# Optimization experiments

Measured on AMD Instinct MI355X. Metric: run time of the kernel, lower is better.

The kernel has to match this reference:

```python
import jax, jax.numpy as jnp
from jax import lax
import numpy as np

S, N, E = 4, 50000, 800000
D_IN, D_NOISE, D_H, D_OUT = 96, 32, 32, 128
F_CAT = D_IN + D_NOISE + D_H  # 160, matches nn.Linear(input_dim+noise_dim+32, out)


def setup_inputs() -> dict:
    key = jax.random.key(0)
    ks = jax.random.split(key, 8)
    X = jax.random.normal(ks[0], (1, N, D_IN), dtype=jnp.float32)
    h = jax.random.normal(ks[1], (1, N, D_H), dtype=jnp.float32)
    # Bernoulli(0.5) noise, sampled in setup for determinism (original samples in forward)
    epsilon = (jax.random.uniform(ks[2], (S, N, D_NOISE)) < 0.5).astype(jnp.float32)
    W = jax.random.normal(ks[3], (F_CAT, D_OUT), dtype=jnp.float32) * 0.02
    b = jnp.zeros((D_OUT,), dtype=jnp.float32)
    gin_eps = jnp.zeros((), dtype=jnp.float32)  # init_eps=0, learn_eps=True
    src = jax.random.randint(ks[4], (E,), 0, N, dtype=jnp.int32)
    dst = jax.random.randint(ks[5], (E,), 0, N, dtype=jnp.int32)
    return {"X": X, "h": h, "epsilon": epsilon, "W": W, "b": b,
            "gin_eps": gin_eps, "src": src, "dst": dst}


def reference(X, h, epsilon, W, b, gin_eps, src, dst):
    # X: [1,N,D_IN] expanded to sample_size; h: [1,N,32] expanded; epsilon: [S,N,D_NOISE]
    s, n = epsilon.shape[0], X.shape[1]
    Xb = jnp.broadcast_to(X, (s, n, X.shape[2]))
    hb = jnp.broadcast_to(h, (s, n, h.shape[2]))
    x_all = jnp.concatenate([Xb, epsilon, hb], axis=2)  # [S,N,F_CAT]

    def per_sample(carry, x):  # x: [N,F_CAT]
        # GINConv('sum'): (1+eps)*x + sum_{j in N(i)} x_j, then Linear, then activation
        agg = (1.0 + gin_eps) * x + jax.ops.segment_sum(x[src], dst, num_segments=n)
        y = jax.nn.relu(agg @ W + b)           # [N,D_OUT]
        return carry, jnp.mean(y, axis=0)      # per-layer mean over nodes -> [D_OUT]

    _, means = lax.scan(per_sample, None, x_all)  # [S,D_OUT]
    # outputTensor[i] = tempdim12 broadcasts the [D_OUT] vector over the node axis
    out = jnp.broadcast_to(means[:, None, :], (s, n, W.shape[1]))
    return jax.nn.relu(out), epsilon
```

## Files before the change

### kernel.cpp

```cpp
#include <hip/hip_runtime.h>

#define N_NODES  50000
#define N_EDGES  800000
#define D_OUTF   128
#define F_PACK   256
#define NTILES   3125
#define GEMM_BLOCKS 512
#define NB1      196
#define PBX 12500
#define PBB 25000
#define PBZ 196
#define PB_TOT (PBX + PBB + PBZ)

typedef __attribute__((ext_vector_type(8))) short bf16x8;
typedef __attribute__((ext_vector_type(4))) float f32x4;

__device__ __forceinline__ unsigned short f2bf(float x) {
  unsigned int u = __float_as_uint(x);
  u += 0x7FFFu + ((u >> 16) & 1u);
  return (unsigned short)(u >> 16);
}
__device__ __forceinline__ float bflo(unsigned int u) { return __uint_as_float(u << 16); }
__device__ __forceinline__ float bfhi(unsigned int u) { return __uint_as_float(u & 0xFFFF0000u); }
__device__ __forceinline__ unsigned int pack2(float a, float b) {
  return (unsigned int)f2bf(a) | ((unsigned int)f2bf(b) << 16);
}
__device__ __forceinline__ unsigned int spreadLo(unsigned int rep) {
  return (((rep & 0x08040201u) + 0x7F7F7F7Fu) >> 7) & 0x01010101u;
}
__device__ __forceinline__ unsigned int spreadHi(unsigned int rep) {
  return (((rep & 0x80402010u) + 0x7F7F7F7Fu) >> 7) & 0x01010101u;
}

__global__ void k_pack(const float* __restrict__ X, const float* __restrict__ h,
                       const float* __restrict__ eps,
                       unsigned int* __restrict__ featXH,
                       unsigned int* __restrict__ epsb, int* __restrict__ cnt) {
  int blk = blockIdx.x, tid = threadIdx.x;
  if (blk < PBX) {
    int t = blk * 256 + tid;
    int node = t >> 6, f = (t & 63) << 1;
    float a, c;
    if (f < 96) { a = X[node * 96 + f];      c = X[node * 96 + f + 1]; }
    else        { a = h[node * 32 + f - 96]; c = h[node * 32 + f - 95]; }
    featXH[t] = pack2(a, c);
  } else if (blk < PBX + PBB) {
    long g = (long)(blk - PBX) * 256 + tid;
    float v = eps[g];
    unsigned long long m = __ballot(v > 0.5f);
    int lane = tid & 63;
    if ((lane & 31) == 0) {
      long idx = g >> 5;
      int s = (int)(idx / N_NODES);
      int node = (int)(idx - (long)s * N_NODES);
      epsb[node * 4 + s] = (unsigned int)(m >> ((lane >> 5) * 32));
    }
  } else {
    int i = (blk - PBX - PBB) * 256 + tid;
    if (i < N_NODES) cnt[i] = 0;
  }
}

__global__ void k_hist(const int* __restrict__ dst, int* __restrict__ cnt) {
  int i = blockIdx.x * blockDim.x + threadIdx.x;
  if (i < N_EDGES) atomicAdd(&cnt[dst[i]], 1);
}

__global__ void k_scan1(const int* __restrict__ cnt, int* __restrict__ excl,
                        int* __restrict__ bsum) {
  __shared__ int wpart[4];
  int tid = threadIdx.x, lane = tid & 63, wid = tid >> 6;
  int i = blockIdx.x * 256 + tid;
  int v = (i < N_NODES) ? cnt[i] : 0;
  int x = v;
#pragma unroll
  for (int d = 1; d < 64; d <<= 1) {
    int t = __shfl_up(x, d, 64);
    if (lane >= d) x += t;
  }
  if (lane == 63) wpart[wid] = x;
  __syncthreads();
  if (tid == 0) {
    int s = 0;
#pragma unroll
    for (int w = 0; w < 4; ++w) { int t = wpart[w]; wpart[w] = s; s += t; }
    bsum[blockIdx.x] = s;
  }
  __syncthreads();
  if (i < N_NODES) excl[i] = wpart[wid] + x - v;
}

__global__ void k_scan2(const int* __restrict__ bsum, int* __restrict__ boff) {
  __shared__ int sd[256];
  int tid = threadIdx.x;
  int v = (tid < NB1) ? bsum[tid] : 0;
  sd[tid] = v;
  __syncthreads();
  for (int d = 1; d < 256; d <<= 1) {
    int t = (tid >= d) ? sd[tid - d] : 0;
    __syncthreads();
    sd[tid] += t;
    __syncthreads();
  }
  if (tid < NB1) boff[tid] = sd[tid] - v;
}

__global__ void k_scan3(int* __restrict__ off, const int* __restrict__ boff,
                        int* __restrict__ cursor) {
  int i = blockIdx.x * 256 + threadIdx.x;
  if (i < N_NODES) {
    int o = off[i] + boff[blockIdx.x];
    off[i] = o;
    cursor[i] = o;
  }
  if (i == 0) off[N_NODES] = N_EDGES;
}

__global__ void k_scatter(const int* __restrict__ src, const int* __restrict__ dst,
                          int* __restrict__ cursor, int* __restrict__ csr) {
  int i = blockIdx.x * blockDim.x + threadIdx.x;
  if (i < N_EDGES) {
    int pos = atomicAdd(&cursor[dst[i]], 1);
    csr[pos] = src[i];
  }
}

__global__ __launch_bounds__(256) void k_agg16(
    const uint4* __restrict__ feat4, const unsigned int* __restrict__ epsw,
    const float* __restrict__ geps_p, const int* __restrict__ off,
    const int* __restrict__ csr, uint4* __restrict__ agg4) {
  int gt = blockIdx.x * blockDim.x + threadIdx.x;
  int n  = gt >> 4;
  int li = gt & 15;
  if (n >= N_NODES) return;
  float ge = 1.0f + geps_p[0];
  int wsel = li >> 2, bsh = (li & 3) * 8;

  uint4 sf = feat4[n * 16 + li];
  float af0 = ge * bflo(sf.x), af1 = ge * bfhi(sf.x);
  float af2 = ge * bflo(sf.y), af3 = ge * bfhi(sf.y);
  float af4 = ge * bflo(sf.z), af5 = ge * bfhi(sf.z);
  float af6 = ge * bflo(sf.w), af7 = ge * bfhi(sf.w);
  unsigned int Bself = (epsw[n * 4 + wsel] >> bsh) & 0xFFu;
  unsigned int accLo = 0, accHi = 0;

  int e = off[n], e1 = off[n + 1];
  for (; e + 1 < e1; e += 2) {
    int s0 = csr[e], s1 = csr[e + 1];
    uint4 f0 = feat4[s0 * 16 + li];
    uint4 f1 = feat4[s1 * 16 + li];
    unsigned int w0 = epsw[s0 * 4 + wsel];
    unsigned int w1 = epsw[s1 * 4 + wsel];
    af0 += bflo(f0.x) + bflo(f1.x);  af1 += bfhi(f0.x) + bfhi(f1.x);
    af2 += bflo(f0.y) + bflo(f1.y);  af3 += bfhi(f0.y) + bfhi(f1.y);
    af4 += bflo(f0.z) + bflo(f1.z);  af5 += bfhi(f0.z) + bfhi(f1.z);
    af6 += bflo(f0.w) + bflo(f1.w);  af7 += bfhi(f0.w) + bfhi(f1.w);
    unsigned int B0 = (w0 >> bsh) & 0xFFu;
    unsigned int B1 = (w1 >> bsh) & 0xFFu;
    unsigned int r0 = B0 | (B0 << 8);  r0 |= r0 << 16;
    unsigned int r1 = B1 | (B1 << 8);  r1 |= r1 << 16;
    accLo += spreadLo(r0) + spreadLo(r1);
    accHi += spreadHi(r0) + spreadHi(r1);
  }
  if (e < e1) {
    int s0 = csr[e];
    uint4 f0 = feat4[s0 * 16 + li];
    unsigned int w0 = epsw[s0 * 4 + wsel];
    af0 += bflo(f0.x); af1 += bfhi(f0.x);
    af2 += bflo(f0.y); af3 += bfhi(f0.y);
    af4 += bflo(f0.z); af5 += bfhi(f0.z);
    af6 += bflo(f0.w); af7 += bfhi(f0.w);
    unsigned int B0 = (w0 >> bsh) & 0xFFu;
    unsigned int r0 = B0 | (B0 << 8);  r0 |= r0 << 16;
    accLo += spreadLo(r0);
    accHi += spreadHi(r0);
  }

  float ev0 = ge * (float)(Bself & 1u)        + (float)(accLo & 0xFFu);
  float ev1 = ge * (float)((Bself >> 1) & 1u) + (float)((accLo >> 8) & 0xFFu);
  float ev2 = ge * (float)((Bself >> 2) & 1u) + (float)((accLo >> 16) & 0xFFu);
  float ev3 = ge * (float)((Bself >> 3) & 1u) + (float)((accLo >> 24) & 0xFFu);
  float ev4 = ge * (float)((Bself >> 4) & 1u) + (float)(accHi & 0xFFu);
  float ev5 = ge * (float)((Bself >> 5) & 1u) + (float)((accHi >> 8) & 0xFFu);
  float ev6 = ge * (float)((Bself >> 6) & 1u) + (float)((accHi >> 16) & 0xFFu);
  float ev7 = ge * (float)((Bself >> 7) & 1u) + (float)((accHi >> 24) & 0xFFu);

  uint4 oXh, oEp;
  oXh.x = pack2(af0, af1); oXh.y = pack2(af2, af3);
  oXh.z = pack2(af4, af5); oXh.w = pack2(af6, af7);
  oEp.x = pack2(ev0, ev1); oEp.y = pack2(ev2, ev3);
  oEp.z = pack2(ev4, ev5); oEp.w = pack2(ev6, ev7);
  agg4[n * 32 + li]      = oXh;
  agg4[n * 32 + 16 + li] = oEp;
}

__global__ __launch_bounds__(256) void k_gemm(const unsigned short* __restrict__ agg,
    const float* __restrict__ W, const float* __restrict__ b,
    float* __restrict__ partials) {
  int tid = threadIdx.x;
  int lane = tid & 63;
  int w = tid >> 6;
  int col = lane & 15;
  int quad = lane >> 4;

  bf16x8 Bsh[2][4];
  bf16x8 Bep[2];
  float bias[2];
#pragma unroll
  for (int i = 0; i < 2; ++i) {
    int obase = (2 * w + i) * 16;
    bias[i] = b[obase + col];
#pragma unroll
    for (int kb = 0; kb < 4; ++kb) {
      bf16x8 f;
#pragma unroll
      for (int j = 0; j < 8; ++j) {
        int k = kb * 32 + quad * 8 + j;
        int wr = (k < 96) ? k : k + 32;
        f[j] = (short)f2bf(W[wr * D_OUTF + obase + col]);
      }
      Bsh[i][kb] = f;
    }
    bf16x8 g;
#pragma unroll
    for (int j = 0; j < 8; ++j)
      g[j] = (short)f2bf(W[(96 + quad * 8 + j) * D_OUTF + obase + col]);
    Bep[i] = g;
  }

  f32x4 psum[4][2];
#pragma unroll
  for (int s = 0; s < 4; ++s)
#pragma unroll
    for (int i = 0; i < 2; ++i) psum[s][i] = (f32x4){0.f, 0.f, 0.f, 0.f};

  for (int t = blockIdx.x; t < NTILES; t += gridDim.x) {
    const unsigned short* arow = agg + (long)(t * 16 + col) * F_PACK;
    bf16x8 Ash[4];
#pragma unroll
    for (int kb = 0; kb < 4; ++kb)
      Ash[kb] = *(const bf16x8*)(arow + kb * 32 + quad * 8);
    f32x4 csh[2];
    csh[0] = (f32x4){0.f, 0.f, 0.f, 0.f};
    csh[1] = (f32x4){0.f, 0.f, 0.f, 0.f};
#pragma unroll
    for (int kb = 0; kb < 4; ++kb) {
      csh[0] = __builtin_amdgcn_mfma_f32_16x16x32_bf16(Ash[kb], Bsh[0][kb], csh[0], 0, 0, 0);
      csh[1] = __builtin_amdgcn_mfma_f32_16x16x32_bf16(Ash[kb], Bsh[1][kb], csh[1], 0, 0, 0);
    }
#pragma unroll
    for (int s = 0; s < 4; ++s) {
      bf16x8 Aep = *(const bf16x8*)(arow + 128 + s * 32 + quad * 8);
#pragma unroll
      for (int i = 0; i < 2; ++i) {
        f32x4 c = __builtin_amdgcn_mfma_f32_16x16x32_bf16(Aep, Bep[i], csh[i], 0, 0, 0);
#pragma unroll
        for (int r = 0; r < 4; ++r)
          psum[s][i][r] += fmaxf(c[r] + bias[i], 0.f);
      }
    }
  }

#pragma unroll
  for (int s = 0; s < 4; ++s)
#pragma unroll
    for (int i = 0; i < 2; ++i) {
      float v = psum[s][i][0] + psum[s][i][1] + psum[s][i][2] + psum[s][i][3];
      v += __shfl_xor(v, 16, 64);
      v += __shfl_xor(v, 32, 64);
      if (quad == 0)
        partials[blockIdx.x * 512 + s * 128 + (2 * w + i) * 16 + col] = v;
    }
}

__global__ void k_reduce(const float* __restrict__ partials, float* __restrict__ means) {
  int idx = blockIdx.x * 64 + threadIdx.x;
  float t = 0.f;
  for (int blk = 0; blk < GEMM_BLOCKS; ++blk) t += partials[blk * 512 + idx];
  means[idx] = fmaxf(t * (1.0f / (float)N_NODES), 0.f);
}

#define OUT0_F4 6400000L
#define EPS_F4  1600000L
__global__ void k_out(const float* __restrict__ means, const float* __restrict__ eps,
                      float* __restrict__ out) {
  long i = (long)blockIdx.x * blockDim.x + threadIdx.x;
  if (i < OUT0_F4) {
    int o4 = (int)(i & 31);
    long sn = i >> 5;
    int s = (int)(sn / N_NODES);
    ((float4*)out)[i] = ((const float4*)means)[s * 32 + o4];
  } else if (i < OUT0_F4 + EPS_F4) {
    long j = i - OUT0_F4;
    ((float4*)out)[OUT0_F4 + j] = ((const float4*)eps)[j];
  }
}

extern "C" void kernel_launch(void* const* d_in, const int* in_sizes, int n_in,
                              void* d_out, int out_size, void* d_ws, size_t ws_size,
                              hipStream_t stream) {
  const float* X    = (const float*)d_in[0];
  const float* h    = (const float*)d_in[1];
  const float* eps  = (const float*)d_in[2];
  const float* W    = (const float*)d_in[3];
  const float* b    = (const float*)d_in[4];
  const float* geps = (const float*)d_in[5];
  const int*   src  = (const int*)d_in[6];
  const int*   dst  = (const int*)d_in[7];
  float* out = (float*)d_out;

  char* w = (char*)d_ws;
  unsigned int*  featXH = (unsigned int*)w;  w += (size_t)N_NODES * 64 * 4;
  unsigned int*  epsb   = (unsigned int*)w;  w += (size_t)N_NODES * 4 * 4;
  unsigned int*  agg_u  = (unsigned int*)w;  w += (size_t)N_NODES * 128 * 4;
  int*   off      = (int*)w;   w += (size_t)(N_NODES + 16) * 4;
  int*   cnt      = (int*)w;   w += (size_t)N_NODES * 4;
  int*   cursor   = (int*)w;   w += (size_t)N_NODES * 4;
  int*   csr      = (int*)w;   w += (size_t)N_EDGES * 4;
  int*   bsum     = (int*)w;   w += 256 * 4;
  int*   boff     = (int*)w;   w += 256 * 4;
  float* partials = (float*)w; w += (size_t)GEMM_BLOCKS * 512 * 4;
  float* means    = (float*)w; w += 512 * 4;

  int eb = (N_EDGES + 255) / 256;
  k_pack<<<PB_TOT, 256, 0, stream>>>(X, h, eps, featXH, epsb, cnt);
  k_hist<<<eb, 256, 0, stream>>>(dst, cnt);
  k_scan1<<<NB1, 256, 0, stream>>>(cnt, off, bsum);
  k_scan2<<<1, 256, 0, stream>>>(bsum, boff);
  k_scan3<<<NB1, 256, 0, stream>>>(off, boff, cursor);
  k_scatter<<<eb, 256, 0, stream>>>(src, dst, cursor, csr);

  k_agg16<<<NTILES, 256, 0, stream>>>((const uint4*)featXH, epsb,
                                      geps, off, csr, (uint4*)agg_u);

  k_gemm<<<GEMM_BLOCKS, 256, 0, stream>>>((const unsigned short*)agg_u, W, b, partials);
  k_reduce<<<8, 64, 0, stream>>>(partials, means);

  long total_f4 = OUT0_F4 + EPS_F4;
  k_out<<<(int)((total_f4 + 255) / 256), 256, 0, stream>>>(means, eps, out);
}
```

Before: 355.1 us.

## Fuse aggregation and MFMA GEMM via LDS, prepack W fragments, parallelize reduce

The GIN aggregation kernel now keeps each 16-node tile of aggregated bf16 features in shared memory and runs the MFMA linear+ReLU+sum directly, so the 25 MB aggregated-feature buffer is no longer written to and re-read from global memory. W is converted to bf16 MFMA fragment layout once in the prep kernel, and every block loads its fragments with vector loads. The reduce step now sums 3125 transposed per-block partials using one wavefront per output with shuffles. The cost is a per-block W fragment reload and a larger partials buffer.

After: 356.2 us. About the same (+0.3%).

```diff
diff --git a/kernel.cpp b/kernel.cpp
--- a/kernel.cpp
+++ b/kernel.cpp
@@ -2,15 +2,14 @@
 
 #define N_NODES  50000
 #define N_EDGES  800000
-#define D_OUTF   128
-#define F_PACK   256
 #define NTILES   3125
-#define GEMM_BLOCKS 512
+#define PT_STRIDE 3200
 #define NB1      196
 #define PBX 12500
 #define PBB 25000
+#define PBW 40
 #define PBZ 196
-#define PB_TOT (PBX + PBB + PBZ)
+#define PB_TOT (PBX + PBB + PBW + PBZ)
 
 typedef __attribute__((ext_vector_type(8))) short bf16x8;
 typedef __attribute__((ext_vector_type(4))) float f32x4;
@@ -32,10 +31,10 @@
   return (((rep & 0x80402010u) + 0x7F7F7F7Fu) >> 7) & 0x01010101u;
 }
 
-__global__ void k_pack(const float* __restrict__ X, const float* __restrict__ h,
-                       const float* __restrict__ eps,
-                       unsigned int* __restrict__ featXH,
-                       unsigned int* __restrict__ epsb, int* __restrict__ cnt) {
+__global__ void k_prep(const float* __restrict__ X, const float* __restrict__ h,
+                       const float* __restrict__ eps, const float* __restrict__ W,
+                       unsigned int* __restrict__ featXH, unsigned int* __restrict__ epsb,
+                       unsigned int* __restrict__ Wfrag, int* __restrict__ cnt) {
   int blk = blockIdx.x, tid = threadIdx.x;
   if (blk < PBX) {
     int t = blk * 256 + tid;
@@ -55,8 +54,25 @@
       int node = (int)(idx - (long)s * N_NODES);
       epsb[node * 4 + s] = (unsigned int)(m >> ((lane >> 5) * 32));
     }
+  } else if (blk < PBX + PBB + PBW) {
+    int u = (blk - PBX - PBB) * 256 + tid;
+    if (u < 10240) {
+      int flat = u * 2;
+      int qj = flat & 31;
+      int c  = (flat >> 5) & 127;
+      int kb = flat >> 12;
+      int q = qj >> 3, j = qj & 7;
+      int wr0;
+      if (kb < 4) {
+        int k = kb * 32 + q * 8 + j;
+        wr0 = (k < 96) ? k : k + 32;
+      } else {
+        wr0 = 96 + q * 8 + j;
+      }
+      Wfrag[u] = pack2(W[wr0 * 128 + c], W[(wr0 + 1) * 128 + c]);
+    }
   } else {
-    int i = (blk - PBX - PBB) * 256 + tid;
+    int i = (blk - PBX - PBB - PBW) * 256 + tid;
     if (i < N_NODES) cnt[i] = 0;
   }
 }
@@ -125,14 +141,18 @@
   }
 }
 
-__global__ __launch_bounds__(256) void k_agg16(
+__global__ __launch_bounds__(256) void k_fused(
     const uint4* __restrict__ feat4, const unsigned int* __restrict__ epsw,
+    const unsigned short* __restrict__ Wf, const float* __restrict__ b,
     const float* __restrict__ geps_p, const int* __restrict__ off,
-    const int* __restrict__ csr, uint4* __restrict__ agg4) {
-  int gt = blockIdx.x * blockDim.x + threadIdx.x;
-  int n  = gt >> 4;
-  int li = gt & 15;
-  if (n >= N_NODES) return;
+    const int* __restrict__ csr, float* __restrict__ partialsT) {
+  __shared__ __align__(16) unsigned short lds[16 * 264];
+  int tid = threadIdx.x;
+  int lane = tid & 63;
+  int w = tid >> 6;
+  int li = tid & 15;
+  int r = tid >> 4;
+  int n = blockIdx.x * 16 + r;
   float ge = 1.0f + geps_p[0];
   int wsel = li >> 2, bsh = (li & 3) * 8;
 
@@ -190,94 +210,59 @@
   oXh.z = pack2(af4, af5); oXh.w = pack2(af6, af7);
   oEp.x = pack2(ev0, ev1); oEp.y = pack2(ev2, ev3);
   oEp.z = pack2(ev4, ev5); oEp.w = pack2(ev6, ev7);
-  agg4[n * 32 + li]      = oXh;
-  agg4[n * 32 + 16 + li] = oEp;
-}
-
-__global__ __launch_bounds__(256) void k_gemm(const unsigned short* __restrict__ agg,
-    const float* __restrict__ W, const float* __restrict__ b,
-    float* __restrict__ partials) {
-  int tid = threadIdx.x;
-  int lane = tid & 63;
-  int w = tid >> 6;
-  int col = lane & 15;
-  int quad = lane >> 4;
-
-  bf16x8 Bsh[2][4];
-  bf16x8 Bep[2];
+  unsigned short* rp = lds + r * 264;
+  *(uint4*)(rp + li * 8) = oXh;
+  *(uint4*)(rp + 128 + li * 8) = oEp;
+  __syncthreads();
+
+  int col = li, quad = lane >> 4;
+  bf16x8 Bsh[2][4], Bep[2];
   float bias[2];
 #pragma unroll
   for (int i = 0; i < 2; ++i) {
-    int obase = (2 * w + i) * 16;
-    bias[i] = b[obase + col];
-#pragma unroll
-    for (int kb = 0; kb < 4; ++kb) {
-      bf16x8 f;
-#pragma unroll
-      for (int j = 0; j < 8; ++j) {
-        int k = kb * 32 + quad * 8 + j;
-        int wr = (k < 96) ? k : k + 32;
-        f[j] = (short)f2bf(W[wr * D_OUTF + obase + col]);
-      }
-      Bsh[i][kb] = f;
-    }
-    bf16x8 g;
-#pragma unroll
-    for (int j = 0; j < 8; ++j)
-      g[j] = (short)f2bf(W[(96 + quad * 8 + j) * D_OUTF + obase + col]);
-    Bep[i] = g;
-  }
-
-  f32x4 psum[4][2];
-#pragma unroll
-  for (int s = 0; s < 4; ++s)
-#pragma unroll
-    for (int i = 0; i < 2; ++i) psum[s][i] = (f32x4){0.f, 0.f, 0.f, 0.f};
-
-  for (int t = blockIdx.x; t < NTILES; t += gridDim.x) {
-    const unsigned short* arow = agg + (long)(t * 16 + col) * F_PACK;
-    bf16x8 Ash[4];
+    int c = (2 * w + i) * 16 + col;
+    bias[i] = b[c];
 #pragma unroll
     for (int kb = 0; kb < 4; ++kb)
-      Ash[kb] = *(const bf16x8*)(arow + kb * 32 + quad * 8);
-    f32x4 csh[2];
-    csh[0] = (f32x4){0.f, 0.f, 0.f, 0.f};
-    csh[1] = (f32x4){0.f, 0.f, 0.f, 0.f};
-#pragma unroll
-    for (int kb = 0; kb < 4; ++kb) {
-      csh[0] = __builtin_amdgcn_mfma_f32_16x16x32_bf16(Ash[kb], Bsh[0][kb], csh[0], 0, 0, 0);
-      csh[1] = __builtin_amdgcn_mfma_f32_16x16x32_bf16(Ash[kb], Bsh[1][kb], csh[1], 0, 0, 0);
-    }
-#pragma unroll
-    for (int s = 0; s < 4; ++s) {
-      bf16x8 Aep = *(const bf16x8*)(arow + 128 + s * 32 + quad * 8);
-#pragma unroll
-      for (int i = 0; i < 2; ++i) {
-        f32x4 c = __builtin_amdgcn_mfma_f32_16x16x32_bf16(Aep, Bep[i], csh[i], 0, 0, 0);
-#pragma unroll
-        for (int r = 0; r < 4; ++r)
-          psum[s][i][r] += fmaxf(c[r] + bias[i], 0.f);
-      }
-    }
-  }
-
-#pragma unroll
-  for (int s = 0; s < 4; ++s)
+      Bsh[i][kb] = *(const bf16x8*)(Wf + (kb * 128 + c) * 32 + quad * 8);
+    Bep[i] = *(const bf16x8*)(Wf + (4 * 128 + c) * 32 + quad * 8);
+  }
+
+  const unsigned short* ap = lds + col * 264;
+  f32x4 csh[2];
+  csh[0] = (f32x4){0.f, 0.f, 0.f, 0.f};
+  csh[1] = (f32x4){0.f, 0.f, 0.f, 0.f};
+#pragma unroll
+  for (int kb = 0; kb < 4; ++kb) {
+    bf16x8 Ash = *(const bf16x8*)(ap + kb * 32 + quad * 8);
+    csh[0] = __builtin_amdgcn_mfma_f32_16x16x32_bf16(Ash, Bsh[0][kb], csh[0], 0, 0, 0);
+    csh[1] = __builtin_amdgcn_mfma_f32_16x16x32_bf16(Ash, Bsh[1][kb], csh[1], 0, 0, 0);
+  }
+#pragma unroll
+  for (int s = 0; s < 4; ++s) {
+    bf16x8 Aep = *(const bf16x8*)(ap + 128 + s * 32 + quad * 8);
 #pragma unroll
     for (int i = 0; i < 2; ++i) {
-      float v = psum[s][i][0] + psum[s][i][1] + psum[s][i][2] + psum[s][i][3];
+      f32x4 c = __builtin_amdgcn_mfma_f32_16x16x32_bf16(Aep, Bep[i], csh[i], 0, 0, 0);
+      float v = fmaxf(c[0] + bias[i], 0.f) + fmaxf(c[1] + bias[i], 0.f)
+              + fmaxf(c[2] + bias[i], 0.f) + fmaxf(c[3] + bias[i], 0.f);
       v += __shfl_xor(v, 16, 64);
       v += __shfl_xor(v, 32, 64);
       if (quad == 0)
-        partials[blockIdx.x * 512 + s * 128 + (2 * w + i) * 16 + col] = v;
+        partialsT[(long)(s * 128 + (2 * w + i) * 16 + col) * PT_STRIDE + blockIdx.x] = v;
     }
-}
-
-__global__ void k_reduce(const float* __restrict__ partials, float* __restrict__ means) {
-  int idx = blockIdx.x * 64 + threadIdx.x;
+  }
+}
+
+__global__ void k_reduce(const float* __restrict__ partialsT, float* __restrict__ means) {
+  int wid = (blockIdx.x * 256 + threadIdx.x) >> 6;
+  int lane = threadIdx.x & 63;
+  const float* row = partialsT + (long)wid * PT_STRIDE;
   float t = 0.f;
-  for (int blk = 0; blk < GEMM_BLOCKS; ++blk) t += partials[blk * 512 + idx];
-  means[idx] = fmaxf(t * (1.0f / (float)N_NODES), 0.f);
+  for (int i = lane; i < NTILES; i += 64) t += row[i];
+#pragma unroll
+  for (int d = 1; d < 64; d <<= 1) t += __shfl_xor(t, d, 64);
+  if (lane == 0) means[wid] = fmaxf(t * (1.0f / (float)N_NODES), 0.f);
 }
 
 #define OUT0_F4 6400000L
@@ -310,31 +295,30 @@
   float* out = (float*)d_out;
 
   char* w = (char*)d_ws;
-  unsigned int*  featXH = (unsigned int*)w;  w += (size_t)N_NODES * 64 * 4;
-  unsigned int*  epsb   = (unsigned int*)w;  w += (size_t)N_NODES * 4 * 4;
-  unsigned int*  agg_u  = (unsigned int*)w;  w += (size_t)N_NODES * 128 * 4;
+  unsigned int* featXH = (unsigned int*)w;  w += (size_t)N_NODES * 64 * 4;
+  unsigned int* epsb   = (unsigned int*)w;  w += (size_t)N_NODES * 4 * 4;
+  unsigned int* Wfrag  = (unsigned int*)w;  w += 10240 * 4;
   int*   off      = (int*)w;   w += (size_t)(N_NODES + 16) * 4;
   int*   cnt      = (int*)w;   w += (size_t)N_NODES * 4;
   int*   cursor   = (int*)w;   w += (size_t)N_NODES * 4;
   int*   csr      = (int*)w;   w += (size_t)N_EDGES * 4;
   int*   bsum     = (int*)w;   w += 256 * 4;
   int*   boff     = (int*)w;   w += 256 * 4;
-  float* partials = (float*)w; w += (size_t)GEMM_BLOCKS * 512 * 4;
+  float* partialsT = (float*)w; w += (size_t)512 * PT_STRIDE * 4;
   float* means    = (float*)w; w += 512 * 4;
 
   int eb = (N_EDGES + 255) / 256;
-  k_pack<<<PB_TOT, 256, 0, stream>>>(X, h, eps, featXH, epsb, cnt);
+  k_prep<<<PB_TOT, 256, 0, stream>>>(X, h, eps, W, featXH, epsb, Wfrag, cnt);
   k_hist<<<eb, 256, 0, stream>>>(dst, cnt);
   k_scan1<<<NB1, 256, 0, stream>>>(cnt, off, bsum);
   k_scan2<<<1, 256, 0, stream>>>(bsum, boff);
   k_scan3<<<NB1, 256, 0, stream>>>(off, boff, cursor);
   k_scatter<<<eb, 256, 0, stream>>>(src, dst, cursor, csr);
 
-  k_agg16<<<NTILES, 256, 0, stream>>>((const uint4*)featXH, epsb,
-                                      geps, off, csr, (uint4*)agg_u);
-
-  k_gemm<<<GEMM_BLOCKS, 256, 0, stream>>>((const unsigned short*)agg_u, W, b, partials);
-  k_reduce<<<8, 64, 0, stream>>>(partials, means);
+  k_fused<<<NTILES, 256, 0, stream>>>((const uint4*)featXH, epsb,
+                                      (const unsigned short*)Wfrag, b, geps,
+                                      off, csr, partialsT);
+  k_reduce<<<128, 256, 0, stream>>>(partialsT, means);
 
   long total_f4 = OUT0_F4 + EPS_F4;
   k_out<<<(int)((total_f4 + 255) / 256), 256, 0, stream>>>(means, eps, out);
```

## Assign one wavefront per node and split its edges across four lane groups

Applied to the files above, without the earlier changes.

The aggregation kernel now gives each node a full 64-lane wavefront instead of 16 lanes. The four 16-lane groups each walk a strided subset of the node's incoming edges, then combine their partial sums with cross-lane xor shuffles. The aim is more parallelism and more memory requests in flight for the gather, which helps nodes with long edge lists. The cost is four times as many threads, extra shuffle work, and idle lanes when a node has few edges (about 16 on average here).

Result: no change. 354.8 us (-0.1%).

```diff
diff --git a/kernel.cpp b/kernel.cpp
--- a/kernel.cpp
+++ b/kernel.cpp
@@ -125,28 +125,29 @@
   }
 }
 
-__global__ __launch_bounds__(256) void k_agg16(
+__global__ __launch_bounds__(256) void k_agg_ep(
     const uint4* __restrict__ feat4, const unsigned int* __restrict__ epsw,
     const float* __restrict__ geps_p, const int* __restrict__ off,
     const int* __restrict__ csr, uint4* __restrict__ agg4) {
-  int gt = blockIdx.x * blockDim.x + threadIdx.x;
-  int n  = gt >> 4;
-  int li = gt & 15;
-  if (n >= N_NODES) return;
+  int wave = (blockIdx.x * blockDim.x + threadIdx.x) >> 6;
+  int lane = threadIdx.x & 63;
+  int li = lane & 15, es = lane >> 4;
+  if (wave >= N_NODES) return;
+  int n = wave;
   float ge = 1.0f + geps_p[0];
   int wsel = li >> 2, bsh = (li & 3) * 8;
 
   uint4 sf = feat4[n * 16 + li];
-  float af0 = ge * bflo(sf.x), af1 = ge * bfhi(sf.x);
-  float af2 = ge * bflo(sf.y), af3 = ge * bfhi(sf.y);
-  float af4 = ge * bflo(sf.z), af5 = ge * bfhi(sf.z);
-  float af6 = ge * bflo(sf.w), af7 = ge * bfhi(sf.w);
-  unsigned int Bself = (epsw[n * 4 + wsel] >> bsh) & 0xFFu;
+  unsigned int swd = epsw[n * 4 + wsel];
+
+  float af0 = 0.f, af1 = 0.f, af2 = 0.f, af3 = 0.f;
+  float af4 = 0.f, af5 = 0.f, af6 = 0.f, af7 = 0.f;
   unsigned int accLo = 0, accHi = 0;
 
-  int e = off[n], e1 = off[n + 1];
-  for (; e + 1 < e1; e += 2) {
-    int s0 = csr[e], s1 = csr[e + 1];
+  int e1 = off[n + 1];
+  int e = off[n] + es;
+  for (; e + 4 < e1; e += 8) {
+    int s0 = csr[e], s1 = csr[e + 4];
     uint4 f0 = feat4[s0 * 16 + li];
     uint4 f1 = feat4[s1 * 16 + li];
     unsigned int w0 = epsw[s0 * 4 + wsel];
@@ -176,22 +177,39 @@
     accHi += spreadHi(r0);
   }
 
-  float ev0 = ge * (float)(Bself & 1u)        + (float)(accLo & 0xFFu);
-  float ev1 = ge * (float)((Bself >> 1) & 1u) + (float)((accLo >> 8) & 0xFFu);
-  float ev2 = ge * (float)((Bself >> 2) & 1u) + (float)((accLo >> 16) & 0xFFu);
-  float ev3 = ge * (float)((Bself >> 3) & 1u) + (float)((accLo >> 24) & 0xFFu);
-  float ev4 = ge * (float)((Bself >> 4) & 1u) + (float)(accHi & 0xFFu);
-  float ev5 = ge * (float)((Bself >> 5) & 1u) + (float)((accHi >> 8) & 0xFFu);
-  float ev6 = ge * (float)((Bself >> 6) & 1u) + (float)((accHi >> 16) & 0xFFu);
-  float ev7 = ge * (float)((Bself >> 7) & 1u) + (float)((accHi >> 24) & 0xFFu);
-
-  uint4 oXh, oEp;
-  oXh.x = pack2(af0, af1); oXh.y = pack2(af2, af3);
-  oXh.z = pack2(af4, af5); oXh.w = pack2(af6, af7);
-  oEp.x = pack2(ev0, ev1); oEp.y = pack2(ev2, ev3);
-  oEp.z = pack2(ev4, ev5); oEp.w = pack2(ev6, ev7);
-  agg4[n * 32 + li]      = oXh;
-  agg4[n * 32 + 16 + li] = oEp;
+#pragma unroll
+  for (int d = 16; d < 64; d <<= 1) {
+    af0 += __shfl_xor(af0, d, 64);  af1 += __shfl_xor(af1, d, 64);
+    af2 += __shfl_xor(af2, d, 64);  af3 += __shfl_xor(af3, d, 64);
+    af4 += __shfl_xor(af4, d, 64);  af5 += __shfl_xor(af5, d, 64);
+    af6 += __shfl_xor(af6, d, 64);  af7 += __shfl_xor(af7, d, 64);
+    accLo += __shfl_xor((int)accLo, d, 64);
+    accHi += __shfl_xor((int)accHi, d, 64);
+  }
+
+  if (es == 0) {
+    af0 += ge * bflo(sf.x);  af1 += ge * bfhi(sf.x);
+    af2 += ge * bflo(sf.y);  af3 += ge * bfhi(sf.y);
+    af4 += ge * bflo(sf.z);  af5 += ge * bfhi(sf.z);
+    af6 += ge * bflo(sf.w);  af7 += ge * bfhi(sf.w);
+    unsigned int Bself = (swd >> bsh) & 0xFFu;
+    float ev0 = ge * (float)(Bself & 1u)        + (float)(accLo & 0xFFu);
+    float ev1 = ge * (float)((Bself >> 1) & 1u) + (float)((accLo >> 8) & 0xFFu);
+    float ev2 = ge * (float)((Bself >> 2) & 1u) + (float)((accLo >> 16) & 0xFFu);
+    float ev3 = ge * (float)((Bself >> 3) & 1u) + (float)((accLo >> 24) & 0xFFu);
+    float ev4 = ge * (float)((Bself >> 4) & 1u) + (float)(accHi & 0xFFu);
+    float ev5 = ge * (float)((Bself >> 5) & 1u) + (float)((accHi >> 8) & 0xFFu);
+    float ev6 = ge * (float)((Bself >> 6) & 1u) + (float)((accHi >> 16) & 0xFFu);
+    float ev7 = ge * (float)((Bself >> 7) & 1u) + (float)((accHi >> 24) & 0xFFu);
+
+    uint4 oXh, oEp;
+    oXh.x = pack2(af0, af1); oXh.y = pack2(af2, af3);
+    oXh.z = pack2(af4, af5); oXh.w = pack2(af6, af7);
+    oEp.x = pack2(ev0, ev1); oEp.y = pack2(ev2, ev3);
+    oEp.z = pack2(ev4, ev5); oEp.w = pack2(ev6, ev7);
+    agg4[n * 32 + li]      = oXh;
+    agg4[n * 32 + 16 + li] = oEp;
+  }
 }
 
 __global__ __launch_bounds__(256) void k_gemm(const unsigned short* __restrict__ agg,
@@ -330,8 +348,8 @@
   k_scan3<<<NB1, 256, 0, stream>>>(off, boff, cursor);
   k_scatter<<<eb, 256, 0, stream>>>(src, dst, cursor, csr);
 
-  k_agg16<<<NTILES, 256, 0, stream>>>((const uint4*)featXH, epsb,
-                                      geps, off, csr, (uint4*)agg_u);
+  k_agg_ep<<<(N_NODES * 64) / 256, 256, 0, stream>>>((const uint4*)featXH, epsb,
+                                                     geps, off, csr, (uint4*)agg_u);
 
   k_gemm<<<GEMM_BLOCKS, 256, 0, stream>>>((const unsigned short*)agg_u, W, b, partials);
   k_reduce<<<8, 64, 0, stream>>>(partials, means);
```
